# Performance work log

Hardware: AMD Instinct MI355X
Metric: run time of the kernel (lower is better)

Reference implementation:

```python
import jax, jax.numpy as jnp
import numpy as np

TEMPERATURE = 0.07
EPS = 1e-8  # torch CosineSimilarity eps


def setup_inputs() -> dict:
    key = jax.random.key(0)
    features = jax.random.normal(key, (16, 1024, 512), dtype=jnp.float32)
    return {"features": features}


def reference(features):
    """Vectorized equivalent of the original double Python loop.

    For each b and each t in [1, T-2]:
      anchor = f[b,t], positive = f[b,t+1]
      negatives = all frames j with j < t-1 or j >= t+2  (excludes t-1, t, t+1)
      loss_bt = -log( exp(cos(a,p)/T) / (exp(cos(a,p)/T) + sum_j exp(cos(a,n_j)/T)) )
    Returns mean over all (b, t) pairs (neg pool is non-empty for all t when T > 3).
    """
    B, T, D = features.shape
    norm = jnp.maximum(jnp.linalg.norm(features, axis=-1, keepdims=True), EPS)
    n = features / norm  # [B, T, D]
    # full pairwise cosine-sim logits, scaled by temperature
    sim = jnp.einsum('btd,bsd->bts', n, n) / TEMPERATURE  # [B, T, T]

    t_idx = jnp.arange(1, T - 1)            # anchors t = 1 .. T-2
    j_idx = jnp.arange(T)
    # negatives: j in [0, t-1) union [t+2, T)  -> excludes t-1, t, t+1
    neg_mask = (j_idx[None, :] < t_idx[:, None] - 1) | (j_idx[None, :] >= t_idx[:, None] + 2)  # [T-2, T]

    logits = sim[:, 1:T - 1, :]                                   # [B, T-2, T]
    pos = logits[:, jnp.arange(T - 2), jnp.arange(2, T)]          # sim[b, t, t+1] -> [B, T-2]
    neg_logits = jnp.where(neg_mask[None], logits, -jnp.inf)
    lse_neg = jax.nn.logsumexp(neg_logits, axis=-1)               # log sum_j exp(neg_sim)
    # -log(exp(pos)/(exp(pos)+negsum)) = logaddexp(pos, lse_neg) - pos
    loss_bt = jnp.logaddexp(pos, lse_neg) - pos                   # [B, T-2]
    return jnp.mean(loss_bt)
```

## Files before the change

### kernel.cpp

```cpp
#include <hip/hip_runtime.h>
#include <hip/hip_fp8.h>

#define B_ 16
#define T_ 1024
#define D_ 512
#define EPS_ 1e-8f
#define SCALE2 20.609929155566063f
#define LN2_ 0.6931471805599453f

#define BT2 128
#define NB2 8
#define NPAIR2 (NB2 * (NB2 + 1) / 2)
#define NKIT 4
#define SCL 0x7B7B7B7B

typedef __attribute__((ext_vector_type(4))) int   int4v;
typedef __attribute__((ext_vector_type(8))) int   int8v;
typedef __attribute__((ext_vector_type(4))) float floatx4;

typedef __attribute__((address_space(1))) const unsigned int g_u32;
typedef __attribute__((address_space(3))) unsigned int l_u32;

__device__ __forceinline__ void glds16(const void* g, void* l) {
    __builtin_amdgcn_global_load_lds((g_u32*)g, (l_u32*)l, 16, 0, 0);
}

__device__ __forceinline__ unsigned char f2e4m3(float x) {
    __hip_fp8_e4m3 q(x);
    return (unsigned char)q.__x;
}

__global__ __launch_bounds__(256) void norm_kernel(const float* __restrict__ f,
                                                   unsigned char* __restrict__ nrm,
                                                   float* __restrict__ rs_g,
                                                   float* __restrict__ rp_g,
                                                   float* __restrict__ out) {
    const int gi = blockIdx.x * 256 + threadIdx.x;
    if (gi < B_ * T_) { rs_g[gi] = 0.0f; rp_g[gi] = 0.0f; }
    if (gi == 0) out[0] = 0.0f;

    const int row  = blockIdx.x * 4 + (threadIdx.x >> 6);
    const int lane = threadIdx.x & 63;
    const size_t off = (size_t)row * D_ + lane * 8;
    const float4 v0 = *(const float4*)(f + off);
    const float4 v1 = *(const float4*)(f + off + 4);
    float ss = v0.x*v0.x + v0.y*v0.y + v0.z*v0.z + v0.w*v0.w
             + v1.x*v1.x + v1.y*v1.y + v1.z*v1.z + v1.w*v1.w;
    #pragma unroll
    for (int o = 32; o >= 1; o >>= 1) ss += __shfl_xor(ss, o, 64);
    const float sc = 16.0f / fmaxf(sqrtf(ss), EPS_);
    unsigned int w0 =  (unsigned int)f2e4m3(v0.x*sc)
                    | ((unsigned int)f2e4m3(v0.y*sc) << 8)
                    | ((unsigned int)f2e4m3(v0.z*sc) << 16)
                    | ((unsigned int)f2e4m3(v0.w*sc) << 24);
    unsigned int w1 =  (unsigned int)f2e4m3(v1.x*sc)
                    | ((unsigned int)f2e4m3(v1.y*sc) << 8)
                    | ((unsigned int)f2e4m3(v1.z*sc) << 16)
                    | ((unsigned int)f2e4m3(v1.w*sc) << 24);
    uint2 w; w.x = w0; w.y = w1;
    *(uint2*)(nrm + (size_t)row * D_ + lane * 8) = w;
}

__global__ __launch_bounds__(256, 2) void loss_kernel(const unsigned char* __restrict__ nrm,
                                                      float* __restrict__ rs_g,
                                                      float* __restrict__ rp_g) {
    const int slot = blockIdx.x & 15;
    int u = blockIdx.x >> 4;
    const int b = ((slot & 7) << 1) | (slot >> 3);
    int bi = 0, rem = NB2;
    while (u >= rem) { u -= rem; --rem; ++bi; }
    const int bj   = bi + u;
    const bool diag = (bi == bj);

    const int t0 = bi * BT2;
    const int j0 = bj * BT2;
    const char* base = (const char*)(nrm + (size_t)b * T_ * D_);

    __shared__ __align__(16) char Ar[4][8192];
    __shared__ __align__(16) char Br[4][8192];

    const int l  = threadIdx.x & 63;
    const int w  = threadIdx.x >> 6;
    const int wr = w >> 1;
    const int wc = w & 1;
    const int m  = l & 15;
    const bool dead = diag && (w == 2);

    const int r   = l >> 2;
    const int gsw = (l & 3) ^ ((r >> 1) & 3);
    const char* sAq[2];
    const char* sBq[2];
    #pragma unroll
    for (int q = 0; q < 2; ++q) {
        sAq[q] = base + (size_t)(t0 + (2 * w + q) * 16 + r) * 512 + gsw * 16;
        sBq[q] = base + (size_t)(j0 + (2 * w + q) * 16 + r) * 512 + gsw * 16;
    }

#define ISSUE(S) do {                                                      \
    _Pragma("unroll")                                                      \
    for (int q_ = 0; q_ < 2; ++q_)                                         \
        glds16(sAq[q_] + (S) * 64, Ar[(S) & 3] + (2 * w + q_) * 1024);     \
    if (!diag) {                                                           \
        _Pragma("unroll")                                                  \
        for (int q_ = 0; q_ < 2; ++q_)                                     \
            glds16(sBq[q_] + (S) * 64, Br[(S) & 3] + (2 * w + q_) * 1024); \
    }                                                                      \
} while (0)

    const int kqh = l >> 5;
    const int ph0 = (2 * ((l >> 4) & 1)) ^ ((m >> 1) & 3);
    const int rd0 = m * 64 + ph0 * 16;
    const int rd1 = m * 64 + (ph0 ^ 1) * 16;

    floatx4 acc[4][4] = {};

    ISSUE(0); ISSUE(1);

    #pragma unroll
    for (int j = 0; j < NKIT; ++j) {
        __syncthreads();
        if (j < NKIT - 1) { ISSUE(2 * j + 2); ISSUE(2 * j + 3); }

        if (!dead) {
            const char* As = Ar[(2 * j + kqh) & 3] + wr * 4096;
            const char* Bs = (diag ? Ar[(2 * j + kqh) & 3] : Br[(2 * j + kqh) & 3]) + wc * 4096;
            int8v af[4], bf[4];
            #pragma unroll
            for (int mi = 0; mi < 4; ++mi) {
                int4v lo = *(const int4v*)(As + mi * 1024 + rd0);
                int4v hi = *(const int4v*)(As + mi * 1024 + rd1);
                af[mi] = __builtin_shufflevector(lo, hi, 0, 1, 2, 3, 4, 5, 6, 7);
            }
            #pragma unroll
            for (int ni = 0; ni < 4; ++ni) {
                int4v lo = *(const int4v*)(Bs + ni * 1024 + rd0);
                int4v hi = *(const int4v*)(Bs + ni * 1024 + rd1);
                bf[ni] = __builtin_shufflevector(lo, hi, 0, 1, 2, 3, 4, 5, 6, 7);
            }
            #pragma unroll
            for (int mi = 0; mi < 4; ++mi)
                #pragma unroll
                for (int ni = 0; ni < 4; ++ni)
                    acc[mi][ni] = __builtin_amdgcn_mfma_scale_f32_16x16x128_f8f6f4(
                        af[mi], bf[ni], acc[mi][ni],
                        0, 0,
                        0, SCL,
                        0, SCL);
        }
    }
#undef ISSUE

    if (dead) return;

    const int t0q = t0 + wr * 64;
    const int j0q = j0 + wc * 64;
    const int d   = t0q - j0q;
    const bool nearq   = (d >= -64 && d <= 62);
    const bool cols_on = !(diag && (wr == wc));
    const int lrow = l >> 4;
    const int lcol = l & 15;
    const int bT   = b * T_;
    float cs[4] = {0.f, 0.f, 0.f, 0.f};

    #pragma unroll
    for (int mi = 0; mi < 4; ++mi) {
        #pragma unroll
        for (int rg = 0; rg < 4; ++rg) {
            const int t = t0q + mi * 16 + lrow * 4 + rg;
            float rsum = 0.f;
            #pragma unroll
            for (int ni = 0; ni < 4; ++ni) {
                const int j  = j0q + ni * 16 + lcol;
                const float s2 = acc[mi][ni][rg] * SCALE2;
                const float e  = exp2f(s2);
                if (j < t - 1 || j > t + 1) { rsum += e; cs[ni] += e; }
                if (nearq && j == t + 1) atomicAdd(&rp_g[bT + t], s2);
            }
            #pragma unroll
            for (int o = 8; o >= 1; o >>= 1) rsum += __shfl_xor(rsum, o, 64);
            if (lcol == 0) atomicAdd(&rs_g[bT + t], rsum);
        }
    }
    if (cols_on) {
        #pragma unroll
        for (int ni = 0; ni < 4; ++ni) {
            float c = cs[ni];
            c += __shfl_xor(c, 16, 64);
            c += __shfl_xor(c, 32, 64);
            if (lrow == 0)
                atomicAdd(&rs_g[bT + j0q + ni * 16 + lcol], c);
        }
    }
}

__global__ __launch_bounds__(256) void fin_kernel(const float* __restrict__ rs_g,
                                                  const float* __restrict__ rp_g,
                                                  float* __restrict__ out) {
    const int idx = blockIdx.x * 256 + threadIdx.x;
    float v = 0.0f;
    if (idx < B_ * T_) {
        const int t = idx & (T_ - 1);
        if (t >= 1 && t <= T_ - 2) {
            const float p2 = rp_g[idx];
            const float s  = rs_g[idx];
            v = (log2f(exp2f(p2) + s) - p2) * LN2_;
        }
    }
    #pragma unroll
    for (int o = 32; o >= 1; o >>= 1) v += __shfl_xor(v, o, 64);
    __shared__ float ws_[4];
    if ((threadIdx.x & 63) == 0) ws_[threadIdx.x >> 6] = v;
    __syncthreads();
    if (threadIdx.x == 0) {
        const float scale = 1.0f / (float)(B_ * (T_ - 2));
        atomicAdd(out, (ws_[0] + ws_[1] + ws_[2] + ws_[3]) * scale);
    }
}

extern "C" void kernel_launch(void* const* d_in, const int* in_sizes, int n_in,
                              void* d_out, int out_size, void* d_ws, size_t ws_size,
                              hipStream_t stream) {
    const float* feat = (const float*)d_in[0];
    float* out = (float*)d_out;

    unsigned char* nrm = (unsigned char*)d_ws;
    float* rs_g = (float*)((char*)d_ws + (size_t)B_ * T_ * D_);
    float* rp_g = rs_g + B_ * T_;

    norm_kernel<<<B_ * T_ / 4, 256, 0, stream>>>(feat, nrm, rs_g, rp_g, out);
    loss_kernel<<<NPAIR2 * B_, 256, 0, stream>>>(nrm, rs_g, rp_g);
    fin_kernel<<<(B_ * T_ + 255) / 256, 256, 0, stream>>>(rs_g, rp_g, out);
}
```

Measured before the change: 93.24 us.

## Fuse norm, loss and finalize into one cooperative persistent kernel

```diff
diff --git a/kernel.cpp b/kernel.cpp
--- a/kernel.cpp
+++ b/kernel.cpp
@@ -1,5 +1,8 @@
 #include <hip/hip_runtime.h>
 #include <hip/hip_fp8.h>
+#include <hip/hip_cooperative_groups.h>
+
+namespace cg = cooperative_groups;
 
 #define B_ 16
 #define T_ 1024
@@ -11,8 +14,10 @@
 #define BT2 128
 #define NB2 8
 #define NPAIR2 (NB2 * (NB2 + 1) / 2)
+#define NJOB (NPAIR2 * B_)
 #define NKIT 4
 #define SCL 0x7B7B7B7B
+#define GRID_ 512
 
 typedef __attribute__((ext_vector_type(4))) int   int4v;
 typedef __attribute__((ext_vector_type(8))) int   int8v;
@@ -30,18 +35,12 @@
     return (unsigned char)q.__x;
 }
 
-__global__ __launch_bounds__(256) void norm_kernel(const float* __restrict__ f,
-                                                   unsigned char* __restrict__ nrm,
-                                                   float* __restrict__ rs_g,
-                                                   float* __restrict__ rp_g,
-                                                   float* __restrict__ out) {
-    const int gi = blockIdx.x * 256 + threadIdx.x;
-    if (gi < B_ * T_) { rs_g[gi] = 0.0f; rp_g[gi] = 0.0f; }
-    if (gi == 0) out[0] = 0.0f;
-
-    const int row  = blockIdx.x * 4 + (threadIdx.x >> 6);
-    const int lane = threadIdx.x & 63;
-    const size_t off = (size_t)row * D_ + lane * 8;
+
+__device__ __forceinline__ void norm_body(const float* __restrict__ f,
+                                          unsigned char* __restrict__ nrm,
+                                          int row) {
+    const int l = threadIdx.x & 63;
+    const size_t off = (size_t)row * D_ + l * 8;
     const float4 v0 = *(const float4*)(f + off);
     const float4 v1 = *(const float4*)(f + off + 4);
     float ss = v0.x*v0.x + v0.y*v0.y + v0.z*v0.z + v0.w*v0.w
@@ -58,14 +57,16 @@
                     | ((unsigned int)f2e4m3(v1.z*sc) << 16)
                     | ((unsigned int)f2e4m3(v1.w*sc) << 24);
     uint2 w; w.x = w0; w.y = w1;
-    *(uint2*)(nrm + (size_t)row * D_ + lane * 8) = w;
-}
-
-__global__ __launch_bounds__(256, 2) void loss_kernel(const unsigned char* __restrict__ nrm,
-                                                      float* __restrict__ rs_g,
-                                                      float* __restrict__ rp_g) {
-    const int slot = blockIdx.x & 15;
-    int u = blockIdx.x >> 4;
+    *(uint2*)(nrm + (size_t)row * D_ + l * 8) = w;
+}
+
+__device__ __forceinline__ void loss_job(const unsigned char* __restrict__ nrm,
+                                         float* __restrict__ rs_g,
+                                         float* __restrict__ rp_g,
+                                         int job,
+                                         char (*Ar)[8192], char (*Br)[8192]) {
+    const int slot = job & 15;
+    int u = job >> 4;
     const int b = ((slot & 7) << 1) | (slot >> 3);
     int bi = 0, rem = NB2;
     while (u >= rem) { u -= rem; --rem; ++bi; }
@@ -76,15 +77,12 @@
     const int j0 = bj * BT2;
     const char* base = (const char*)(nrm + (size_t)b * T_ * D_);
 
-    __shared__ __align__(16) char Ar[4][8192];
-    __shared__ __align__(16) char Br[4][8192];
-
     const int l  = threadIdx.x & 63;
-    const int w  = threadIdx.x >> 6;
-    const int wr = w >> 1;
-    const int wc = w & 1;
+    const int wv = threadIdx.x >> 6;
+    const int wr = wv >> 1;
+    const int wc = wv & 1;
     const int m  = l & 15;
-    const bool dead = diag && (w == 2);
+    const bool dead = diag && (wv == 2);
 
     const int r   = l >> 2;
     const int gsw = (l & 3) ^ ((r >> 1) & 3);
@@ -92,19 +90,19 @@
     const char* sBq[2];
     #pragma unroll
     for (int q = 0; q < 2; ++q) {
-        sAq[q] = base + (size_t)(t0 + (2 * w + q) * 16 + r) * 512 + gsw * 16;
-        sBq[q] = base + (size_t)(j0 + (2 * w + q) * 16 + r) * 512 + gsw * 16;
-    }
-
-#define ISSUE(S) do {                                                      \
-    _Pragma("unroll")                                                      \
-    for (int q_ = 0; q_ < 2; ++q_)                                         \
-        glds16(sAq[q_] + (S) * 64, Ar[(S) & 3] + (2 * w + q_) * 1024);     \
-    if (!diag) {                                                           \
-        _Pragma("unroll")                                                  \
-        for (int q_ = 0; q_ < 2; ++q_)                                     \
-            glds16(sBq[q_] + (S) * 64, Br[(S) & 3] + (2 * w + q_) * 1024); \
-    }                                                                      \
+        sAq[q] = base + (size_t)(t0 + (2 * wv + q) * 16 + r) * 512 + gsw * 16;
+        sBq[q] = base + (size_t)(j0 + (2 * wv + q) * 16 + r) * 512 + gsw * 16;
+    }
+
+#define ISSUE(S) do {                                                       \
+    _Pragma("unroll")                                                       \
+    for (int q_ = 0; q_ < 2; ++q_)                                          \
+        glds16(sAq[q_] + (S) * 64, Ar[(S) & 3] + (2 * wv + q_) * 1024);     \
+    if (!diag) {                                                            \
+        _Pragma("unroll")                                                   \
+        for (int q_ = 0; q_ < 2; ++q_)                                      \
+            glds16(sBq[q_] + (S) * 64, Br[(S) & 3] + (2 * wv + q_) * 1024); \
+    }                                                                       \
 } while (0)
 
     const int kqh = l >> 5;
@@ -123,7 +121,8 @@
 
         if (!dead) {
             const char* As = Ar[(2 * j + kqh) & 3] + wr * 4096;
-            const char* Bs = (diag ? Ar[(2 * j + kqh) & 3] : Br[(2 * j + kqh) & 3]) + wc * 4096;
+            const char* Bs = (diag ? Ar[(2 * j + kqh) & 3]
+                                   : Br[(2 * j + kqh) & 3]) + wc * 4096;
             int8v af[4], bf[4];
             #pragma unroll
             for (int mi = 0; mi < 4; ++mi) {
@@ -191,6 +190,79 @@
                 atomicAdd(&rs_g[bT + j0q + ni * 16 + lcol], c);
         }
     }
+}
+
+__global__ __launch_bounds__(256, 2) void fused_kernel(const float* __restrict__ f,
+                                                       unsigned char* __restrict__ nrm,
+                                                       float* __restrict__ rs_g,
+                                                       float* __restrict__ rp_g,
+                                                       float* __restrict__ out) {
+    cg::grid_group grid = cg::this_grid();
+
+    __shared__ __align__(16) char Ar[4][8192];
+    __shared__ __align__(16) char Br[4][8192];
+    __shared__ float fs_[4];
+
+    const int tid = threadIdx.x;
+    const int l   = tid & 63;
+    const int wv  = tid >> 6;
+
+    {
+        const int gi = blockIdx.x * 256 + tid;
+        if (gi < B_ * T_) { rs_g[gi] = 0.0f; rp_g[gi] = 0.0f; }
+        if (gi == 0) out[0] = 0.0f;
+        for (int row = blockIdx.x * 4 + wv; row < B_ * T_; row += GRID_ * 4)
+            norm_body(f, nrm, row);
+    }
+
+    grid.sync();
+
+    for (int job = blockIdx.x; job < NJOB; job += GRID_) {
+        __syncthreads();
+        loss_job(nrm, rs_g, rp_g, job, Ar, Br);
+    }
+
+    grid.sync();
+
+    {
+        const int idx = blockIdx.x * 256 + tid;
+        float v = 0.0f;
+        if (idx < B_ * T_) {
+            const int t = idx & (T_ - 1);
+            if (t >= 1 && t <= T_ - 2) {
+                const float p2 = rp_g[idx];
+                const float s  = rs_g[idx];
+                v = (log2f(exp2f(p2) + s) - p2) * LN2_;
+            }
+        }
+        #pragma unroll
+        for (int o = 32; o >= 1; o >>= 1) v += __shfl_xor(v, o, 64);
+        if (l == 0) fs_[wv] = v;
+        __syncthreads();
+        if (tid == 0 && blockIdx.x < (B_ * T_ + 255) / 256) {
+            const float scale = 1.0f / (float)(B_ * (T_ - 2));
+            atomicAdd(out, (fs_[0] + fs_[1] + fs_[2] + fs_[3]) * scale);
+        }
+    }
+}
+
+__global__ __launch_bounds__(256) void norm_kernel(const float* __restrict__ f,
+                                                   unsigned char* __restrict__ nrm,
+                                                   float* __restrict__ rs_g,
+                                                   float* __restrict__ rp_g,
+                                                   float* __restrict__ out) {
+    const int gi = blockIdx.x * 256 + threadIdx.x;
+    if (gi < B_ * T_) { rs_g[gi] = 0.0f; rp_g[gi] = 0.0f; }
+    if (gi == 0) out[0] = 0.0f;
+    norm_body(f, nrm, blockIdx.x * 4 + (threadIdx.x >> 6));
+}
+
+__global__ __launch_bounds__(256, 2) void loss_kernel(const unsigned char* __restrict__ nrm,
+                                                      float* __restrict__ rs_g,
+                                                      float* __restrict__ rp_g) {
+    __shared__ __align__(16) char Ar[4][8192];
+    __shared__ __align__(16) char Br[4][8192];
+    loss_job(nrm, rs_g, rp_g, blockIdx.x, Ar, Br);
 }
 
 __global__ __launch_bounds__(256) void fin_kernel(const float* __restrict__ rs_g,
@@ -227,7 +299,14 @@
     float* rs_g = (float*)((char*)d_ws + (size_t)B_ * T_ * D_);
     float* rp_g = rs_g + B_ * T_;
 
-    norm_kernel<<<B_ * T_ / 4, 256, 0, stream>>>(feat, nrm, rs_g, rp_g, out);
-    loss_kernel<<<NPAIR2 * B_, 256, 0, stream>>>(nrm, rs_g, rp_g);
-    fin_kernel<<<(B_ * T_ + 255) / 256, 256, 0, stream>>>(rs_g, rp_g, out);
-}
+    void* args[] = { (void*)&feat, (void*)&nrm, (void*)&rs_g, (void*)&rp_g,
+                     (void*)&out };
+    hipError_t err = hipLaunchCooperativeKernel((const void*)fused_kernel,
+                                                dim3(GRID_), dim3(256),
+                                                args, 0, stream);
+    if (err != hipSuccess) {
+        norm_kernel<<<B_ * T_ / 4, 256, 0, stream>>>(feat, nrm, rs_g, rp_g, out);
+        loss_kernel<<<NJOB, 256, 0, stream>>>(nrm, rs_g, rp_g);
+        fin_kernel<<<(B_ * T_ + 255) / 256, 256, 0, stream>>>(rs_g, rp_g, out);
+    }
+}
```

Result: slower. 200.4 us (+115.0%).

## Replace float atomics with per-column-block partial buffers reduced in finalizer

Applied to the files above, without the earlier changes.

```diff
diff --git a/kernel.cpp b/kernel.cpp
--- a/kernel.cpp
+++ b/kernel.cpp
@@ -11,6 +11,7 @@
 #define BT2 128
 #define NB2 8
 #define NPAIR2 (NB2 * (NB2 + 1) / 2)
+#define NJOB (NPAIR2 * B_)
 #define NKIT 4
 #define SCL 0x7B7B7B7B
 
@@ -32,12 +33,8 @@
 
 __global__ __launch_bounds__(256) void norm_kernel(const float* __restrict__ f,
                                                    unsigned char* __restrict__ nrm,
-                                                   float* __restrict__ rs_g,
-                                                   float* __restrict__ rp_g,
                                                    float* __restrict__ out) {
-    const int gi = blockIdx.x * 256 + threadIdx.x;
-    if (gi < B_ * T_) { rs_g[gi] = 0.0f; rp_g[gi] = 0.0f; }
-    if (gi == 0) out[0] = 0.0f;
+    if (blockIdx.x == 0 && threadIdx.x == 0) out[0] = 0.0f;
 
     const int row  = blockIdx.x * 4 + (threadIdx.x >> 6);
     const int lane = threadIdx.x & 63;
@@ -62,7 +59,7 @@
 }
 
 __global__ __launch_bounds__(256, 2) void loss_kernel(const unsigned char* __restrict__ nrm,
-                                                      float* __restrict__ rs_g,
+                                                      float* __restrict__ P,
                                                       float* __restrict__ rp_g) {
     const int slot = blockIdx.x & 15;
     int u = blockIdx.x >> 4;
@@ -80,11 +77,11 @@
     __shared__ __align__(16) char Br[4][8192];
 
     const int l  = threadIdx.x & 63;
-    const int w  = threadIdx.x >> 6;
-    const int wr = w >> 1;
-    const int wc = w & 1;
+    const int wv = threadIdx.x >> 6;
+    const int wr = wv >> 1;
+    const int wc = wv & 1;
     const int m  = l & 15;
-    const bool dead = diag && (w == 2);
+    const bool dead = diag && (wv == 2);
 
     const int r   = l >> 2;
     const int gsw = (l & 3) ^ ((r >> 1) & 3);
@@ -92,19 +89,19 @@
     const char* sBq[2];
     #pragma unroll
     for (int q = 0; q < 2; ++q) {
-        sAq[q] = base + (size_t)(t0 + (2 * w + q) * 16 + r) * 512 + gsw * 16;
-        sBq[q] = base + (size_t)(j0 + (2 * w + q) * 16 + r) * 512 + gsw * 16;
-    }
-
-#define ISSUE(S) do {                                                      \
-    _Pragma("unroll")                                                      \
-    for (int q_ = 0; q_ < 2; ++q_)                                         \
-        glds16(sAq[q_] + (S) * 64, Ar[(S) & 3] + (2 * w + q_) * 1024);     \
-    if (!diag) {                                                           \
-        _Pragma("unroll")                                                  \
-        for (int q_ = 0; q_ < 2; ++q_)                                     \
-            glds16(sBq[q_] + (S) * 64, Br[(S) & 3] + (2 * w + q_) * 1024); \
-    }                                                                      \
+        sAq[q] = base + (size_t)(t0 + (2 * wv + q) * 16 + r) * 512 + gsw * 16;
+        sBq[q] = base + (size_t)(j0 + (2 * wv + q) * 16 + r) * 512 + gsw * 16;
+    }
+
+#define ISSUE(S) do {                                                       \
+    _Pragma("unroll")                                                       \
+    for (int q_ = 0; q_ < 2; ++q_)                                          \
+        glds16(sAq[q_] + (S) * 64, Ar[(S) & 3] + (2 * wv + q_) * 1024);     \
+    if (!diag) {                                                            \
+        _Pragma("unroll")                                                   \
+        for (int q_ = 0; q_ < 2; ++q_)                                      \
+            glds16(sBq[q_] + (S) * 64, Br[(S) & 3] + (2 * wv + q_) * 1024); \
+    }                                                                       \
 } while (0)
 
     const int kqh = l >> 5;
@@ -123,7 +120,8 @@
 
         if (!dead) {
             const char* As = Ar[(2 * j + kqh) & 3] + wr * 4096;
-            const char* Bs = (diag ? Ar[(2 * j + kqh) & 3] : Br[(2 * j + kqh) & 3]) + wc * 4096;
+            const char* Bs = (diag ? Ar[(2 * j + kqh) & 3]
+                                   : Br[(2 * j + kqh) & 3]) + wc * 4096;
             int8v af[4], bf[4];
             #pragma unroll
             for (int mi = 0; mi < 4; ++mi) {
@@ -160,6 +158,8 @@
     const int lrow = l >> 4;
     const int lcol = l & 15;
     const int bT   = b * T_;
+    float* Pr = P + (size_t)(2 * bj + wc) * (B_ * T_) + bT;
+    float* Pc = P + (size_t)(2 * bi + wr) * (B_ * T_) + bT;
     float cs[4] = {0.f, 0.f, 0.f, 0.f};
 
     #pragma unroll
@@ -174,11 +174,11 @@
                 const float s2 = acc[mi][ni][rg] * SCALE2;
                 const float e  = exp2f(s2);
                 if (j < t - 1 || j > t + 1) { rsum += e; cs[ni] += e; }
-                if (nearq && j == t + 1) atomicAdd(&rp_g[bT + t], s2);
+                if (nearq && j == t + 1) rp_g[bT + t] = s2;
             }
             #pragma unroll
             for (int o = 8; o >= 1; o >>= 1) rsum += __shfl_xor(rsum, o, 64);
-            if (lcol == 0) atomicAdd(&rs_g[bT + t], rsum);
+            if (lcol == 0) Pr[t] = rsum;
         }
     }
     if (cols_on) {
@@ -187,13 +187,12 @@
             float c = cs[ni];
             c += __shfl_xor(c, 16, 64);
             c += __shfl_xor(c, 32, 64);
-            if (lrow == 0)
-                atomicAdd(&rs_g[bT + j0q + ni * 16 + lcol], c);
-        }
-    }
-}
-
-__global__ __launch_bounds__(256) void fin_kernel(const float* __restrict__ rs_g,
+            if (lrow == 0) Pc[j0q + ni * 16 + lcol] = c;
+        }
+    }
+}
+
+__global__ __launch_bounds__(256) void fin_kernel(const float* __restrict__ P,
                                                   const float* __restrict__ rp_g,
                                                   float* __restrict__ out) {
     const int idx = blockIdx.x * 256 + threadIdx.x;
@@ -201,8 +200,10 @@
     if (idx < B_ * T_) {
         const int t = idx & (T_ - 1);
         if (t >= 1 && t <= T_ - 2) {
+            float s = 0.0f;
+            #pragma unroll
+            for (int p = 0; p < 16; ++p) s += P[(size_t)p * (B_ * T_) + idx];
             const float p2 = rp_g[idx];
-            const float s  = rs_g[idx];
             v = (log2f(exp2f(p2) + s) - p2) * LN2_;
         }
     }
@@ -224,10 +225,10 @@
     float* out = (float*)d_out;
 
     unsigned char* nrm = (unsigned char*)d_ws;
-    float* rs_g = (float*)((char*)d_ws + (size_t)B_ * T_ * D_);
-    float* rp_g = rs_g + B_ * T_;
-
-    norm_kernel<<<B_ * T_ / 4, 256, 0, stream>>>(feat, nrm, rs_g, rp_g, out);
-    loss_kernel<<<NPAIR2 * B_, 256, 0, stream>>>(nrm, rs_g, rp_g);
-    fin_kernel<<<(B_ * T_ + 255) / 256, 256, 0, stream>>>(rs_g, rp_g, out);
-}
+    float* P    = (float*)((char*)d_ws + (size_t)B_ * T_ * D_);
+    float* rp_g = P + 16 * (B_ * T_);
+
+    norm_kernel<<<B_ * T_ / 4, 256, 0, stream>>>(feat, nrm, out);
+    loss_kernel<<<NJOB, 256, 0, stream>>>(nrm, P, rp_g);
+    fin_kernel<<<(B_ * T_ + 255) / 256, 256, 0, stream>>>(P, rp_g, out);
+}
```

Measured after the change: 93.62 us. No clear change (+0.4%).
